# Kernel optimization log

Hardware: AMD Instinct MI355X
Metric: run time of the kernel (lower is better)

## Reference

```python
import jax, jax.numpy as jnp
import numpy as np

STRIDES = (2, 2, 1)   # module init arg: (2,2,1) per docstring example
EPS = 1e-5            # InstanceNorm epsilon
ALPHA = 0.2           # leaky relu slope
DN = ('NDHWC', 'DHWIO', 'NDHWC')


def setup_inputs() -> dict:
    key = jax.random.key(0)
    k1, k2 = jax.random.split(key, 2)
    # x: [B, D, H, W, Cin] NDHWC volume batch
    x = jax.random.normal(k1, (4, 128, 128, 32, 32), dtype=jnp.float32)
    # w: per-sample hypernetwork kernels [B, kD, kH, kW, Cin, Cout]
    w = jax.random.normal(k2, (4, 3, 3, 3, 32, 64), dtype=jnp.float32) * 0.05
    # InstanceNorm affine params (learned)
    gamma = jnp.ones((64,), dtype=jnp.float32)
    beta = jnp.zeros((64,), dtype=jnp.float32)
    return {"x": x, "w": w, "gamma": gamma, "beta": beta}


def _per_sample_conv(xi, wi):
    # xi: [D,H,W,Cin], wi: [kD,kH,kW,Cin,Cout] -> [D',H',W',Cout]
    return jax.lax.conv_general_dilated(
        xi[None], wi, window_strides=STRIDES, padding='SAME',
        dimension_numbers=DN)[0]


def reference(x, w, gamma, beta):
    # batched dynamic conv: distinct kernel per sample, vectorized via vmap
    y = jax.vmap(_per_sample_conv)(x, w)          # [B, D', H', W', Cout]
    # InstanceNorm: normalize over spatial dims per sample, per channel
    mu = jnp.mean(y, axis=(1, 2, 3), keepdims=True)
    var = jnp.var(y, axis=(1, 2, 3), keepdims=True)
    y = (y - mu) * jax.lax.rsqrt(var + EPS) * gamma + beta
    # leaky relu alpha=0.2
    return jnp.where(y >= 0, y, ALPHA * y)
```

## Files before the change

### kernel.cpp

```cpp
#include <hip/hip_runtime.h>
#include <hip/hip_bf16.h>

#define B_ 4
#define D_ 128
#define H_ 128
#define W_ 32
#define CI 32
#define CO 64
#define OD 64
#define OH 64
#define OW 32
#define S_SPATIAL (OD*OH*OW)
#define EPS 1e-5f
#define ALPHA 0.2f

#define XR 9
#define XC 34
#define UNITS (4*XR*XC)
#define SLICEB (UNITS*16)
#define PLANEF (H_*W_*CI)

typedef __attribute__((ext_vector_type(8))) short short8;
typedef __attribute__((ext_vector_type(4))) float f32x4;

__device__ inline short f2bf(float f) {
    return __builtin_bit_cast(short, __float2bfloat16(f));
}

__device__ inline short8 pack8(float4 a, float4 b) {
    short8 r;
    r[0]=f2bf(a.x); r[1]=f2bf(a.y); r[2]=f2bf(a.z); r[3]=f2bf(a.w);
    r[4]=f2bf(b.x); r[5]=f2bf(b.y); r[6]=f2bf(b.z); r[7]=f2bf(b.w);
    return r;
}

__global__ __launch_bounds__(512) void zero_ws_kernel(float* ws) {
    ws[threadIdx.x] = 0.f;
}

__global__ __launch_bounds__(64) void wprep_kernel(const float* __restrict__ w,
                                                   short* __restrict__ wp) {
    int blk = blockIdx.x;
    int nf  = blk & 3;
    int tb  = blk >> 2;
    int l   = threadIdx.x;
    int l15 = l & 15, lhi = l >> 4;
    const float* wsrc = w + (size_t)tb * (CI*CO);
    short8 v;
#pragma unroll
    for (int j = 0; j < 8; ++j)
        v[j] = f2bf(wsrc[(lhi*8 + j)*CO + nf*16 + l15]);
    *(short8*)(wp + (size_t)blk*512 + l*8) = v;
}

#define ISSUE(plane) \
    _Pragma("unroll") for (int k = 0; k < 5; ++k) { \
        if (soff[k] >= 0) { \
            la[k] = *(const float4*)((plane) + soff[k]); \
            lb[k] = *(const float4*)((plane) + soff[k] + 4); \
        } else { \
            la[k] = make_float4(0.f,0.f,0.f,0.f); \
            lb[k] = la[k]; \
        } }

#define WRITEB(base) \
    _Pragma("unroll") for (int k = 0; k < 5; ++k) { \
        int U_ = t + (k << 8); \
        if (U_ < UNITS) *(short8*)((base) + U_*16) = pack8(la[k], lb[k]); }

#define BARRIER_KEEP_VMEM() \
    asm volatile("s_waitcnt lgkmcnt(0)" ::: "memory"); \
    __builtin_amdgcn_s_barrier(); \
    __builtin_amdgcn_sched_barrier(0)

__global__ __launch_bounds__(256, 4) void conv_mfma_kernel(const float* __restrict__ x,
                                                           const short* __restrict__ wp,
                                                           float* __restrict__ out,
                                                           float* __restrict__ ws) {
    const int bid = blockIdx.x;
    const int b   = bid >> 10;
    const int od  = (bid >> 4) & 63;
    const int oh0 = (bid & 15) << 2;
    const int t   = threadIdx.x;
    const int wv  = t >> 6;
    const int l   = t & 63;
    const int l15 = l & 15;
    const int lhi = l >> 4;

    const float* xb  = x + (size_t)b * (D_*PLANEF);
    const short* wpb = wp + (size_t)b * (27*2048);

    __shared__ __align__(16) char smem[2*SLICEB];
    char* buf0 = smem;
    char* buf1 = smem + SLICEB;

    int soff[5];
#pragma unroll
    for (int k = 0; k < 5; ++k) {
        int U   = t + (k << 8);
        int g   = U / (XR*XC);
        int rem = U % (XR*XC);
        int r   = rem / XC;
        int c   = rem % XC;
        int ih  = oh0*2 + r;
        int iw  = c - 1;
        soff[k] = (U < UNITS && ih < H_ && (unsigned)iw < (unsigned)W_)
                    ? (ih*(W_*CI) + iw*CI + g*8) : -1;
    }

    f32x4 acc[2][4];
#pragma unroll
    for (int mf = 0; mf < 2; ++mf)
#pragma unroll
        for (int nf = 0; nf < 4; ++nf)
            acc[mf][nf] = (f32x4){0.f, 0.f, 0.f, 0.f};

    auto compute = [&](int kd, const char* base) {
        const short* wkd = wpb + (size_t)kd*(9*2048) + l*8;
#pragma unroll
        for (int kh = 0; kh < 3; ++kh) {
            const int r = 2*wv + kh;
#pragma unroll
            for (int kw = 0; kw < 3; ++kw) {
                const short* wpt = wkd + (kh*3 + kw)*2048;
                short8 bf0 = *(const short8*)(wpt);
                short8 bf1 = *(const short8*)(wpt + 512);
                short8 bf2 = *(const short8*)(wpt + 1024);
                short8 bf3 = *(const short8*)(wpt + 1536);
#pragma unroll
                for (int mf = 0; mf < 2; ++mf) {
                    int c = mf*16 + l15 + kw;
                    int U = (lhi*XR + r)*XC + c;
                    short8 a = *(const short8*)(base + U*16);
                    acc[mf][0] = __builtin_amdgcn_mfma_f32_16x16x32_bf16(a, bf0, acc[mf][0], 0,0,0);
                    acc[mf][1] = __builtin_amdgcn_mfma_f32_16x16x32_bf16(a, bf1, acc[mf][1], 0,0,0);
                    acc[mf][2] = __builtin_amdgcn_mfma_f32_16x16x32_bf16(a, bf2, acc[mf][2], 0,0,0);
                    acc[mf][3] = __builtin_amdgcn_mfma_f32_16x16x32_bf16(a, bf3, acc[mf][3], 0,0,0);
                }
            }
        }
    };

    const int id0 = od*2;
    const float* p0 = xb + (size_t)id0 * PLANEF;
    const float* p1 = p0 + PLANEF;
    const bool has2 = (id0 + 2) < D_;
    const float* p2 = has2 ? (p1 + PLANEF) : p1;

    float4 la[5], lb[5];

    ISSUE(p0);
    WRITEB(buf0);
    ISSUE(p1);
    BARRIER_KEEP_VMEM();

    compute(0, buf0);
    WRITEB(buf1);
    BARRIER_KEEP_VMEM();

    ISSUE(p2);
    __builtin_amdgcn_sched_barrier(0);
    compute(1, buf1);
    WRITEB(buf0);
    BARRIER_KEEP_VMEM();

    if (has2) compute(2, buf0);

    const int oh = oh0 + wv;
    float* yb = out + (size_t)((b*OD + od)*OH + oh) * (OW*CO);
#pragma unroll
    for (int mf = 0; mf < 2; ++mf)
#pragma unroll
        for (int nf = 0; nf < 4; ++nf)
#pragma unroll
            for (int r = 0; r < 4; ++r) {
                int ow = mf*16 + lhi*4 + r;
                int co = nf*16 + l15;
                yb[ow*CO + co] = acc[mf][nf][r];
            }

    __syncthreads();
    float* lsum = (float*)smem;
    float* lsq  = (float*)(smem + 1024);
    float csum[4], csq[4];
#pragma unroll
    for (int nf = 0; nf < 4; ++nf) {
        float s = 0.f, q = 0.f;
#pragma unroll
        for (int mf = 0; mf < 2; ++mf)
#pragma unroll
            for (int r = 0; r < 4; ++r) {
                float v = acc[mf][nf][r];
                s += v;
                q = fmaf(v, v, q);
            }
        s += __shfl_xor(s, 16, 64); s += __shfl_xor(s, 32, 64);
        q += __shfl_xor(q, 16, 64); q += __shfl_xor(q, 32, 64);
        csum[nf] = s; csq[nf] = q;
    }
    if (lhi == 0) {
#pragma unroll
        for (int nf = 0; nf < 4; ++nf) {
            lsum[wv*64 + nf*16 + l15] = csum[nf];
            lsq[wv*64 + nf*16 + l15]  = csq[nf];
        }
    }
    __syncthreads();
    if (t < 64) {
        float s = lsum[t] + lsum[64 + t] + lsum[128 + t] + lsum[192 + t];
        float q = lsq[t]  + lsq[64 + t]  + lsq[128 + t]  + lsq[192 + t];
        atomicAdd(&ws[b*64 + t], s);
        atomicAdd(&ws[256 + b*64 + t], q);
    }
}

__global__ __launch_bounds__(256) void finalize_kernel(float* ws,
                                                       const float* __restrict__ gamma,
                                                       const float* __restrict__ beta) {
    int t = threadIdx.x;
    int co = t & 63;
    const float invS = 1.0f / (float)S_SPATIAL;
    float sum = ws[t];
    float sq  = ws[256 + t];
    float mu  = sum * invS;
    float var = sq * invS - mu*mu;
    float scale = rsqrtf(var + EPS) * gamma[co];
    ws[512 + t] = scale;
    ws[768 + t] = beta[co] - mu*scale;
}

__global__ __launch_bounds__(256) void norm_kernel(float* __restrict__ y,
                                                   const float* __restrict__ ws) {
    size_t i = (size_t)blockIdx.x * 256 + threadIdx.x;
    int b = (int)(i >> 21);
    const float4* scp = (const float4*)(ws + 512 + b*64);
    const float4* shp = (const float4*)(ws + 768 + b*64);
    float4 sc = scp[i & 15];
    float4 sh = shp[i & 15];
    float4 v = ((const float4*)y)[i];
    float4 r;
    r.x = fmaf(v.x, sc.x, sh.x);
    r.y = fmaf(v.y, sc.y, sh.y);
    r.z = fmaf(v.z, sc.z, sh.z);
    r.w = fmaf(v.w, sc.w, sh.w);
    r.x = r.x >= 0.f ? r.x : ALPHA * r.x;
    r.y = r.y >= 0.f ? r.y : ALPHA * r.y;
    r.z = r.z >= 0.f ? r.z : ALPHA * r.z;
    r.w = r.w >= 0.f ? r.w : ALPHA * r.w;
    ((float4*)y)[i] = r;
}

extern "C" void kernel_launch(void* const* d_in, const int* in_sizes, int n_in,
                              void* d_out, int out_size, void* d_ws, size_t ws_size,
                              hipStream_t stream) {
    const float* x     = (const float*)d_in[0];
    const float* w     = (const float*)d_in[1];
    const float* gamma = (const float*)d_in[2];
    const float* beta  = (const float*)d_in[3];
    float* out = (float*)d_out;
    float* ws  = (float*)d_ws;
    short* wp  = (short*)((char*)d_ws + 4096);

    zero_ws_kernel<<<1, 512, 0, stream>>>(ws);
    wprep_kernel<<<B_*27*4, 64, 0, stream>>>(w, wp);
    conv_mfma_kernel<<<B_*OD*(OH/4), 256, 0, stream>>>(x, wp, out, ws);
    finalize_kernel<<<1, 256, 0, stream>>>(ws, gamma, beta);
    norm_kernel<<<32768, 256, 0, stream>>>(out, ws);
}
```

Before: 247.3 us.

## Stage weights into LDS via direct global-to-LDS loads, single-buffer input

Each kd slice of the per-sample weights is now copied into shared memory with global_load_lds, and the MFMA loop reads B fragments from LDS rather than from global memory. The input slice goes from double-buffered to a single buffer, so each stage waits for its loads before computing and loads no longer overlap compute. LDS use rises (about 19.6KB plus 36KB), and launch bounds drop from 4 to 2 blocks per CU, which lowers occupancy. The aim is to cut repeated global and L2 traffic for weights, at the cost of a serialized load/compute schedule.

```diff
diff --git a/kernel.cpp b/kernel.cpp
--- a/kernel.cpp
+++ b/kernel.cpp
@@ -17,7 +17,8 @@
 #define XR 9
 #define XC 34
 #define UNITS (4*XR*XC)
-#define SLICEB (UNITS*16)
+#define XSLICEB (UNITS*16)
+#define WSLICEB (9*4096)
 #define PLANEF (H_*W_*CI)
 
 typedef __attribute__((ext_vector_type(8))) short short8;
@@ -32,6 +33,12 @@
     r[0]=f2bf(a.x); r[1]=f2bf(a.y); r[2]=f2bf(a.z); r[3]=f2bf(a.w);
     r[4]=f2bf(b.x); r[5]=f2bf(b.y); r[6]=f2bf(b.z); r[7]=f2bf(b.w);
     return r;
+}
+
+__device__ inline void gload16(const void* g, const void* l) {
+    __builtin_amdgcn_global_load_lds(
+        (const __attribute__((address_space(1))) void*)g,
+        (__attribute__((address_space(3))) void*)l, 16, 0, 0);
 }
 
 __global__ __launch_bounds__(512) void zero_ws_kernel(float* ws) {
@@ -53,27 +60,17 @@
     *(short8*)(wp + (size_t)blk*512 + l*8) = v;
 }
 
-#define ISSUE(plane) \
-    _Pragma("unroll") for (int k = 0; k < 5; ++k) { \
-        if (soff[k] >= 0) { \
-            la[k] = *(const float4*)((plane) + soff[k]); \
-            lb[k] = *(const float4*)((plane) + soff[k] + 4); \
-        } else { \
-            la[k] = make_float4(0.f,0.f,0.f,0.f); \
-            lb[k] = la[k]; \
-        } }
-
-#define WRITEB(base) \
-    _Pragma("unroll") for (int k = 0; k < 5; ++k) { \
-        int U_ = t + (k << 8); \
-        if (U_ < UNITS) *(short8*)((base) + U_*16) = pack8(la[k], lb[k]); }
-
-#define BARRIER_KEEP_VMEM() \
+#define BARRIER_FULL() \
+    asm volatile("s_waitcnt vmcnt(0) lgkmcnt(0)" ::: "memory"); \
+    __builtin_amdgcn_s_barrier(); \
+    __builtin_amdgcn_sched_barrier(0)
+
+#define BARRIER_LGKM() \
     asm volatile("s_waitcnt lgkmcnt(0)" ::: "memory"); \
     __builtin_amdgcn_s_barrier(); \
     __builtin_amdgcn_sched_barrier(0)
 
-__global__ __launch_bounds__(256, 4) void conv_mfma_kernel(const float* __restrict__ x,
+__global__ __launch_bounds__(256, 2) void conv_mfma_kernel(const float* __restrict__ x,
                                                            const short* __restrict__ wp,
                                                            float* __restrict__ out,
                                                            float* __restrict__ ws) {
@@ -90,9 +87,9 @@
     const float* xb  = x + (size_t)b * (D_*PLANEF);
     const short* wpb = wp + (size_t)b * (27*2048);
 
-    __shared__ __align__(16) char smem[2*SLICEB];
-    char* buf0 = smem;
-    char* buf1 = smem + SLICEB;
+    __shared__ __align__(16) char smem[XSLICEB + WSLICEB];
+    char* xbuf = smem;
+    char* wbuf = smem + XSLICEB;
 
     int soff[5];
 #pragma unroll
@@ -115,23 +112,47 @@
         for (int nf = 0; nf < 4; ++nf)
             acc[mf][nf] = (f32x4){0.f, 0.f, 0.f, 0.f};
 
-    auto compute = [&](int kd, const char* base) {
-        const short* wkd = wpb + (size_t)kd*(9*2048) + l*8;
+    auto stage = [&](const float* plane, int kd) {
+        const short* wsrc = wpb + (size_t)kd * (9*2048);
+#pragma unroll
+        for (int k = 0; k < 9; ++k) {
+            int u = t + (k << 8);
+            gload16(wsrc + u*8, wbuf + u*16);
+        }
+        float4 la[5], lb[5];
+#pragma unroll
+        for (int k = 0; k < 5; ++k) {
+            if (soff[k] >= 0) {
+                la[k] = *(const float4*)(plane + soff[k]);
+                lb[k] = *(const float4*)(plane + soff[k] + 4);
+            } else {
+                la[k] = make_float4(0.f,0.f,0.f,0.f);
+                lb[k] = la[k];
+            }
+        }
+#pragma unroll
+        for (int k = 0; k < 5; ++k) {
+            int U = t + (k << 8);
+            if (U < UNITS) *(short8*)(xbuf + U*16) = pack8(la[k], lb[k]);
+        }
+    };
+
+    auto compute = [&]() {
 #pragma unroll
         for (int kh = 0; kh < 3; ++kh) {
             const int r = 2*wv + kh;
 #pragma unroll
             for (int kw = 0; kw < 3; ++kw) {
-                const short* wpt = wkd + (kh*3 + kw)*2048;
+                const char* wpt = wbuf + (kh*3 + kw)*4096 + l*16;
                 short8 bf0 = *(const short8*)(wpt);
-                short8 bf1 = *(const short8*)(wpt + 512);
-                short8 bf2 = *(const short8*)(wpt + 1024);
-                short8 bf3 = *(const short8*)(wpt + 1536);
+                short8 bf1 = *(const short8*)(wpt + 1024);
+                short8 bf2 = *(const short8*)(wpt + 2048);
+                short8 bf3 = *(const short8*)(wpt + 3072);
 #pragma unroll
                 for (int mf = 0; mf < 2; ++mf) {
                     int c = mf*16 + l15 + kw;
                     int U = (lhi*XR + r)*XC + c;
-                    short8 a = *(const short8*)(base + U*16);
+                    short8 a = *(const short8*)(xbuf + U*16);
                     acc[mf][0] = __builtin_amdgcn_mfma_f32_16x16x32_bf16(a, bf0, acc[mf][0], 0,0,0);
                     acc[mf][1] = __builtin_amdgcn_mfma_f32_16x16x32_bf16(a, bf1, acc[mf][1], 0,0,0);
                     acc[mf][2] = __builtin_amdgcn_mfma_f32_16x16x32_bf16(a, bf2, acc[mf][2], 0,0,0);
@@ -147,24 +168,17 @@
     const bool has2 = (id0 + 2) < D_;
     const float* p2 = has2 ? (p1 + PLANEF) : p1;
 
-    float4 la[5], lb[5];
-
-    ISSUE(p0);
-    WRITEB(buf0);
-    ISSUE(p1);
-    BARRIER_KEEP_VMEM();
-
-    compute(0, buf0);
-    WRITEB(buf1);
-    BARRIER_KEEP_VMEM();
-
-    ISSUE(p2);
-    __builtin_amdgcn_sched_barrier(0);
-    compute(1, buf1);
-    WRITEB(buf0);
-    BARRIER_KEEP_VMEM();
-
-    if (has2) compute(2, buf0);
+    stage(p0, 0);
+    BARRIER_FULL();
+    compute();
+    BARRIER_LGKM();
+    stage(p1, 1);
+    BARRIER_FULL();
+    compute();
+    BARRIER_LGKM();
+    stage(p2, 2);
+    BARRIER_FULL();
+    if (has2) compute();
 
     const int oh = oh0 + wv;
     float* yb = out + (size_t)((b*OD + od)*OH + oh) * (OW*CO);
```

Result: faster. 242.4 us (-2.0%).
